# Optimization experiments

Measured on AMD Instinct MI355X. Metric: run time of the kernel, lower is better.

The kernel has to match this reference:

```python
import jax, jax.numpy as jnp
import numpy as np

K = 16      # knn neighbors (init kwarg k)
EPS = 1e-5  # batch-norm eps


def setup_inputs() -> dict:
    key = jax.random.key(0)
    ks = jax.random.split(key, 4)
    B, N, C, O = 16, 2048, 16, 64
    x = jax.random.normal(ks[0], (B * N, C), dtype=jnp.float32)
    batch = jnp.repeat(jnp.arange(B, dtype=jnp.int32), N)  # sorted equal-size graphs
    W1 = jax.random.normal(ks[1], (2 * C, O), dtype=jnp.float32) * (1.0 / np.sqrt(2 * C))
    b1 = jnp.zeros((O,), jnp.float32)
    g1 = jnp.ones((O,), jnp.float32)
    be1 = jnp.zeros((O,), jnp.float32)
    Wg = jax.random.normal(ks[2], (O, 1), dtype=jnp.float32) * (1.0 / np.sqrt(O))
    bg = jnp.zeros((1,), jnp.float32)
    gg = jnp.ones((1,), jnp.float32)
    beg = jnp.zeros((1,), jnp.float32)
    return {"x": x, "batch": batch, "W1": W1, "b1": b1, "g1": g1, "be1": be1,
            "Wg": Wg, "bg": bg, "gg": gg, "beg": beg, "num_graphs": B}


def reference(x, batch, W1, b1, g1, be1, Wg, bg, gg, beg, num_graphs):
    B = int(num_graphs)
    total, C = x.shape
    N = total // B
    xb = x.reshape(B, N, C)

    # --- dynamic kNN graph in feature space (per graph in the batch) ---
    sq = jnp.sum(xb * xb, axis=-1)                                   # [B,N]
    d = sq[:, :, None] + sq[:, None, :] - 2.0 * jnp.einsum('bnc,bmc->bnm', xb, xb)
    _, idx = jax.lax.top_k(-d, K)                                    # [B,N,K], includes self (d=0)

    # --- edge features: cat([x_i, x_j - x_i]) ---
    xj = jax.vmap(lambda pts, ids: pts[ids])(xb, idx)                # [B,N,K,C]
    xi = jnp.broadcast_to(xb[:, :, None, :], xj.shape)               # [B,N,K,C]
    e = jnp.concatenate([xi, xj - xi], axis=-1)                      # [B,N,K,2C]

    # --- edge MLP: Linear -> BatchNorm(train stats) -> SiLU ---
    h = e @ W1 + b1                                                  # [B,N,K,O]
    mu = h.mean(axis=(0, 1, 2))
    var = h.var(axis=(0, 1, 2))
    h = jax.nn.silu((h - mu) / jnp.sqrt(var + EPS) * g1 + be1)

    # --- attentional aggregation: gate MLP -> softmax over k edges -> weighted sum ---
    gt = h @ Wg + bg                                                 # [B,N,K,1]
    gmu = gt.mean()
    gvar = gt.var()
    gt = jax.nn.silu((gt - gmu) / jnp.sqrt(gvar + EPS) * gg + beg)
    a = jax.nn.softmax(gt, axis=2)                                   # softmax over K per target node
    out = jnp.sum(a * h, axis=2)                                     # [B,N,O]
    return out.reshape(total, -1)
```

## Files before the change

kernel.cpp:

```cpp
#include <hip/hip_runtime.h>
#include <math.h>
#include <float.h>

#define BGRAPH 16
#define NPTS   2048
#define CDIM   16
#define ODIM   64
#define KNN    16
#define NTOT   (BGRAPH*NPTS)
#define NEDGE  (NTOT*KNN)
#define EPSBN  1e-5f
#define NBLK_E 2048
#define NPW    4
#define NSETS  16


__global__ __launch_bounds__(256) void pq_kernel(
    const float* __restrict__ x, const float* __restrict__ W1,
    const float* __restrict__ b1,
    float* __restrict__ P, float* __restrict__ Q, float* __restrict__ sq,
    float* __restrict__ abuf) {
  if (blockIdx.x == 0) {
    for (int t = threadIdx.x; t < NSETS*128 + 2*NSETS; t += 256) abuf[t] = 0.f;
  }
  int lane = threadIdx.x & 63;
  int nin  = threadIdx.x >> 6;
  int node = blockIdx.x * 4 + nin;
  __shared__ float xs[4][CDIM];
  if (threadIdx.x < 4*CDIM) {
    int n = threadIdx.x / CDIM, c = threadIdx.x % CDIM;
    xs[n][c] = x[(blockIdx.x*4 + n)*CDIM + c];
  }
  __syncthreads();
  float p = 0.f, q = b1[lane];
  #pragma unroll
  for (int c = 0; c < CDIM; ++c) {
    float xv = xs[nin][c];
    float wb = W1[(c+CDIM)*ODIM + lane];
    float wa = W1[c*ODIM + lane];
    p += xv * wb;
    q += xv * (wa - wb);
  }
  P[node*ODIM + lane] = p;
  Q[node*ODIM + lane] = q;
  if (lane == 0) {
    float s = 0.f;
    #pragma unroll
    for (int c = 0; c < CDIM; ++c) { float xv = xs[nin][c]; s += xv*xv; }
    sq[node] = s;
  }
}

#define KROWS 4
__device__ __forceinline__ unsigned long long packkey(float dv, int j) {
  unsigned ub = __float_as_uint(dv);
  ub ^= ((unsigned)((int)ub >> 31)) | 0x80000000u;
  return (((unsigned long long)ub) << 32) | (unsigned)j;
}

__global__ __launch_bounds__(256, 4) void knn_kernel(
    const float* __restrict__ x, const float* __restrict__ sq,
    int* __restrict__ idxOut) {
  __shared__ float sT16[CDIM][256];
  __shared__ unsigned long long skey[4][64];
  __shared__ int scnt[4];
  const int tid  = threadIdx.x;
  const int lane = tid & 63;
  const int w    = tid >> 6;
  const int blocksPerGraph = NPTS / KROWS;
  const int g     = blockIdx.x / blocksPerGraph;
  const int rb    = (blockIdx.x % blocksPerGraph) * KROWS;
  const int gbase = g * NPTS;
  const int r0    = rb + w;

  float tg[CDIM]; float tsq;
  {
    const float4* tp = (const float4*)(x + (size_t)(gbase + r0)*CDIM);
    float4 t0 = tp[0], t1 = tp[1], t2 = tp[2], t3 = tp[3];
    tg[0]=t0.x; tg[1]=t0.y; tg[2]=t0.z; tg[3]=t0.w;
    tg[4]=t1.x; tg[5]=t1.y; tg[6]=t1.z; tg[7]=t1.w;
    tg[8]=t2.x; tg[9]=t2.y; tg[10]=t2.z; tg[11]=t2.w;
    tg[12]=t3.x; tg[13]=t3.y; tg[14]=t3.z; tg[15]=t3.w;
    tsq = sq[gbase + r0];
  }

  float d[32];

  float4 a0, a1, a2, a3;
  {
    const float4* xp = (const float4*)(x + (size_t)(gbase + tid)*CDIM);
    a0 = xp[0]; a1 = xp[1]; a2 = xp[2]; a3 = xp[3];
  }

  for (int t = 0; t < NPTS/256; ++t) {
    __syncthreads();
    sT16[0][tid]=a0.x;  sT16[1][tid]=a0.y;  sT16[2][tid]=a0.z;  sT16[3][tid]=a0.w;
    sT16[4][tid]=a1.x;  sT16[5][tid]=a1.y;  sT16[6][tid]=a1.z;  sT16[7][tid]=a1.w;
    sT16[8][tid]=a2.x;  sT16[9][tid]=a2.y;  sT16[10][tid]=a2.z; sT16[11][tid]=a2.w;
    sT16[12][tid]=a3.x; sT16[13][tid]=a3.y; sT16[14][tid]=a3.z; sT16[15][tid]=a3.w;
    __syncthreads();
    if (t < NPTS/256 - 1) {
      const float4* xp = (const float4*)(x + (size_t)(gbase + (t+1)*256 + tid)*CDIM);
      a0 = xp[0]; a1 = xp[1]; a2 = xp[2]; a3 = xp[3];
    }

    float4 sq4 = *(const float4*)(sq + gbase + t*256 + 4*lane);
    float sqv[4] = {sq4.x, sq4.y, sq4.z, sq4.w};

    float dot[4] = {0.f,0.f,0.f,0.f};
    #pragma unroll
    for (int c = 0; c < CDIM; ++c) {
      float4 cv = *(const float4*)(&sT16[c][4*lane]);
      float cvv[4]; cvv[0]=cv.x; cvv[1]=cv.y; cvv[2]=cv.z; cvv[3]=cv.w;
      float xv = tg[c];
      #pragma unroll
      for (int rr = 0; rr < 4; ++rr)
        dot[rr] += xv * cvv[rr];
    }
    #pragma unroll
    for (int rr = 0; rr < 4; ++rr)
      d[t*4 + rr] = tsq + sqv[rr] - 2.f*dot[rr];
  }

  {
    float lmin = d[0];
    #pragma unroll
    for (int s = 1; s < 32; ++s) lmin = fminf(lmin, d[s]);

    float v = lmin;
    #pragma unroll
    for (int k = 2; k <= 64; k <<= 1) {
      #pragma unroll
      for (int j = k >> 1; j > 0; j >>= 1) {
        float o = __shfl_xor(v, j);
        bool asc   = ((lane & k) == 0);
        bool lower = ((lane & j) == 0);
        float mn = fminf(v, o), mx = fmaxf(v, o);
        v = (asc == lower) ? mn : mx;
      }
    }
    float T = __shfl(v, 15);

    if (lane == 0) scnt[w] = 0;
    #pragma unroll
    for (int s = 0; s < 32; ++s) {
      if (d[s] <= T) {
        int p = atomicAdd(&scnt[w], 1);
        if (p < 64) {
          int j = (s >> 2)*256 + 4*lane + (s & 3);
          skey[w][p] = packkey(d[s], j);
        }
      }
    }
    int M = scnt[w];
    int row = gbase + r0;

    if (M <= 64) {
      unsigned long long key = (lane < M) ? skey[w][lane] : ~0ull;
      #pragma unroll
      for (int k = 2; k <= 64; k <<= 1) {
        #pragma unroll
        for (int j = k >> 1; j > 0; j >>= 1) {
          unsigned long long o = __shfl_xor(key, j);
          bool asc   = ((lane & k) == 0);
          bool lower = ((lane & j) == 0);
          unsigned long long mn = (key < o) ? key : o;
          unsigned long long mx = (key < o) ? o : key;
          key = (asc == lower) ? mn : mx;
        }
      }
      if (lane < KNN)
        idxOut[(size_t)row*KNN + lane] = gbase + (int)(key & 0xffffffffu);
    } else {
      for (int sel = 0; sel < KNN; ++sel) {
        unsigned long long lb = ~0ull;
        #pragma unroll
        for (int s = 0; s < 32; ++s) {
          int j = (s >> 2)*256 + 4*lane + (s & 3);
          unsigned long long ks = packkey(d[s], j);
          if (ks < lb) lb = ks;
        }
        #pragma unroll
        for (int off = 32; off > 0; off >>= 1) {
          unsigned long long o = __shfl_xor(lb, off);
          if (o < lb) lb = o;
        }
        if (lane == 0)
          idxOut[(size_t)row*KNN + sel] = gbase + (int)(lb & 0xffffffffu);
        #pragma unroll
        for (int s = 0; s < 32; ++s) {
          int j = (s >> 2)*256 + 4*lane + (s & 3);
          if (packkey(d[s], j) == lb) d[s] = FLT_MAX;
        }
      }
    }
  }
}

__global__ __launch_bounds__(256) void stats1a_kernel(
    const float* __restrict__ P, const float* __restrict__ Q,
    const int* __restrict__ idx, float* __restrict__ abuf) {
  int tid  = threadIdx.x;
  int lane = tid & 63;
  int wid  = tid >> 6;
  int grp  = lane >> 4;
  int p    = lane & 15;
  int gw   = blockIdx.x * 4 + wid;
  int n0 = gw * NPW;
  float4 s4  = {0.f,0.f,0.f,0.f};
  float4 ss4 = {0.f,0.f,0.f,0.f};
  #pragma unroll
  for (int ii = 0; ii < NPW; ++ii) {
    int i = n0 + ii;
    float4 q4 = *(const float4*)(Q + (size_t)i*ODIM + 4*p);
    int4 j4 = *(const int4*)(idx + (size_t)i*KNN + 4*grp);
    {
      float4 v = *(const float4*)(P + (size_t)j4.x*ODIM + 4*p);
      float hx=q4.x+v.x, hy=q4.y+v.y, hz=q4.z+v.z, hw=q4.w+v.w;
      s4.x+=hx; s4.y+=hy; s4.z+=hz; s4.w+=hw;
      ss4.x+=hx*hx; ss4.y+=hy*hy; ss4.z+=hz*hz; ss4.w+=hw*hw;
    }
    {
      float4 v = *(const float4*)(P + (size_t)j4.y*ODIM + 4*p);
      float hx=q4.x+v.x, hy=q4.y+v.y, hz=q4.z+v.z, hw=q4.w+v.w;
      s4.x+=hx; s4.y+=hy; s4.z+=hz; s4.w+=hw;
      ss4.x+=hx*hx; ss4.y+=hy*hy; ss4.z+=hz*hz; ss4.w+=hw*hw;
    }
    {
      float4 v = *(const float4*)(P + (size_t)j4.z*ODIM + 4*p);
      float hx=q4.x+v.x, hy=q4.y+v.y, hz=q4.z+v.z, hw=q4.w+v.w;
      s4.x+=hx; s4.y+=hy; s4.z+=hz; s4.w+=hw;
      ss4.x+=hx*hx; ss4.y+=hy*hy; ss4.z+=hz*hz; ss4.w+=hw*hw;
    }
    {
      float4 v = *(const float4*)(P + (size_t)j4.w*ODIM + 4*p);
      float hx=q4.x+v.x, hy=q4.y+v.y, hz=q4.z+v.z, hw=q4.w+v.w;
      s4.x+=hx; s4.y+=hy; s4.z+=hz; s4.w+=hw;
      ss4.x+=hx*hx; ss4.y+=hy*hy; ss4.z+=hz*hz; ss4.w+=hw*hw;
    }
  }
  s4.x  += __shfl_xor(s4.x,16);  s4.x  += __shfl_xor(s4.x,32);
  s4.y  += __shfl_xor(s4.y,16);  s4.y  += __shfl_xor(s4.y,32);
  s4.z  += __shfl_xor(s4.z,16);  s4.z  += __shfl_xor(s4.z,32);
  s4.w  += __shfl_xor(s4.w,16);  s4.w  += __shfl_xor(s4.w,32);
  ss4.x += __shfl_xor(ss4.x,16); ss4.x += __shfl_xor(ss4.x,32);
  ss4.y += __shfl_xor(ss4.y,16); ss4.y += __shfl_xor(ss4.y,32);
  ss4.z += __shfl_xor(ss4.z,16); ss4.z += __shfl_xor(ss4.z,32);
  ss4.w += __shfl_xor(ss4.w,16); ss4.w += __shfl_xor(ss4.w,32);
  __shared__ float ls[4][ODIM], lss[4][ODIM];
  if (grp == 0) {
    *(float4*)&ls[wid][4*p]  = s4;
    *(float4*)&lss[wid][4*p] = ss4;
  }
  __syncthreads();
  if (tid < 2*ODIM) {
    float a;
    if (tid < ODIM) a = ls[0][tid] + ls[1][tid] + ls[2][tid] + ls[3][tid];
    else { int o = tid - ODIM; a = lss[0][o] + lss[1][o] + lss[2][o] + lss[3][o]; }
    atomicAdd(&abuf[(blockIdx.x & (NSETS-1))*128 + tid], a);
  }
}

__global__ __launch_bounds__(256) void stats2a_kernel(
    const float* __restrict__ P, const float* __restrict__ Q,
    const int* __restrict__ idx,
    const float* __restrict__ g1, const float* __restrict__ be1,
    const float* __restrict__ Wg, const float* __restrict__ bg,
    const float* __restrict__ abuf, float* __restrict__ scale,
    float* __restrict__ shift, float* __restrict__ gtbuf,
    float* __restrict__ gacc) {
  int tid  = threadIdx.x;
  int lane = tid & 63;
  int wid  = tid >> 6;
  int grp  = lane >> 4;
  int p    = lane & 15;
  __shared__ __align__(16) float s_sc[ODIM], s_sh[ODIM];
  __shared__ float red[2*ODIM];
  if (tid < 2*ODIM) {
    float a = 0.f;
    #pragma unroll
    for (int t = 0; t < NSETS; ++t) a += abuf[t*128 + tid];
    red[tid] = a;
  }
  __syncthreads();
  if (tid < ODIM) {
    float mu  = red[tid] / (float)NEDGE;
    float var = red[ODIM+tid] / (float)NEDGE - mu*mu;
    float inv = 1.0f / sqrtf(var + EPSBN);
    float sc = g1[tid] * inv;
    float sh = be1[tid] - mu * sc;
    s_sc[tid] = sc; s_sh[tid] = sh;
    if (blockIdx.x == 0) { scale[tid] = sc; shift[tid] = sh; }
  }
  __syncthreads();

  int gw = blockIdx.x * 4 + wid;
  int n0 = gw * NPW;
  float4 sc4 = *(const float4*)&s_sc[4*p];
  float4 sh4 = *(const float4*)&s_sh[4*p];
  float4 wg4 = *(const float4*)(Wg + 4*p);
  float bgv = bg[0];
  float s = 0.f, ss = 0.f;
  #pragma unroll
  for (int ii = 0; ii < NPW; ++ii) {
    int i = n0 + ii;
    float4 q4 = *(const float4*)(Q + (size_t)i*ODIM + 4*p);
    int4 j4 = *(const int4*)(idx + (size_t)i*KNN + 4*grp);
    #pragma unroll
    for (int e = 0; e < 4; ++e) {
      int j = (e==0) ? j4.x : (e==1) ? j4.y : (e==2) ? j4.z : j4.w;
      float4 p4 = *(const float4*)(P + (size_t)j*ODIM + 4*p);
      float zx = (q4.x + p4.x)*sc4.x + sh4.x;
      float zy = (q4.y + p4.y)*sc4.y + sh4.y;
      float zz = (q4.z + p4.z)*sc4.z + sh4.z;
      float zw = (q4.w + p4.w)*sc4.w + sh4.w;
      float v = (zx/(1.f+expf(-zx)))*wg4.x
              + (zy/(1.f+expf(-zy)))*wg4.y
              + (zz/(1.f+expf(-zz)))*wg4.z
              + (zw/(1.f+expf(-zw)))*wg4.w;
      v += __shfl_xor(v, 1);
      v += __shfl_xor(v, 2);
      v += __shfl_xor(v, 4);
      v += __shfl_xor(v, 8);
      float gt = v + bgv;
      if (p == 0) gtbuf[(size_t)i*KNN + 4*grp + e] = gt;
      s += gt; ss += gt*gt;
    }
  }
  s  += __shfl_xor(s, 16);  s  += __shfl_xor(s, 32);
  ss += __shfl_xor(ss, 16); ss += __shfl_xor(ss, 32);
  __shared__ float pw[4], pws[4];
  if (lane == 0) { pw[wid] = s; pws[wid] = ss; }
  __syncthreads();
  if (tid == 0) {
    int set = blockIdx.x & (NSETS-1);
    atomicAdd(&gacc[2*set],   pw[0]+pw[1]+pw[2]+pw[3]);
    atomicAdd(&gacc[2*set+1], pws[0]+pws[1]+pws[2]+pws[3]);
  }
}

__global__ __launch_bounds__(256) void final_kernel(
    const float* __restrict__ P, const float* __restrict__ Q,
    const int* __restrict__ idx, const float* __restrict__ scale,
    const float* __restrict__ shift, const float* __restrict__ gtbuf,
    const float* __restrict__ gacc, const float* __restrict__ gg,
    const float* __restrict__ beg, float* __restrict__ out) {
  __shared__ float g2[2];
  if (threadIdx.x == 0) {
    float S = 0.f, SS = 0.f;
    #pragma unroll
    for (int t = 0; t < NSETS; ++t) { S += gacc[2*t]; SS += gacc[2*t+1]; }
    float mu  = S / (float)NEDGE;
    float var = SS / (float)NEDGE - mu*mu;
    float inv = 1.f / sqrtf(var + EPSBN);
    float sg = gg[0] * inv;
    g2[0] = sg; g2[1] = beg[0] - mu * sg;
  }
  __syncthreads();
  int lane = threadIdx.x & 63;
  int wid  = threadIdx.x >> 6;
  int grp  = lane >> 4;
  int p    = lane & 15;
  int i = blockIdx.x * 4 + wid;
  float4 sc4 = *(const float4*)(scale + 4*p);
  float4 sh4 = *(const float4*)(shift + 4*p);
  float gscale = g2[0], gshift = g2[1];
  float4 q4 = *(const float4*)(Q + (size_t)i*ODIM + 4*p);
  int4   j4 = *(const int4*)(idx + (size_t)i*KNN + 4*grp);
  float4 g4 = *(const float4*)(gtbuf + (size_t)i*KNN + 4*grp);

  float z0 = g4.x*gscale + gshift, z1 = g4.y*gscale + gshift;
  float z2 = g4.z*gscale + gshift, z3 = g4.w*gscale + gshift;
  float gt0 = z0/(1.f+expf(-z0)), gt1 = z1/(1.f+expf(-z1));
  float gt2 = z2/(1.f+expf(-z2)), gt3 = z3/(1.f+expf(-z3));
  float m = fmaxf(fmaxf(gt0, gt1), fmaxf(gt2, gt3));
  m = fmaxf(m, __shfl_xor(m, 16));
  m = fmaxf(m, __shfl_xor(m, 32));
  float e0 = expf(gt0-m), e1 = expf(gt1-m), e2 = expf(gt2-m), e3 = expf(gt3-m);
  float se = e0+e1+e2+e3;
  se += __shfl_xor(se, 16);
  se += __shfl_xor(se, 32);
  float invs = 1.f / se;
  float a0 = e0*invs, a1 = e1*invs, a2 = e2*invs, a3 = e3*invs;

  float4 acc = {0.f,0.f,0.f,0.f};
  {
    float4 v = *(const float4*)(P + (size_t)j4.x*ODIM + 4*p);
    float zx=(q4.x+v.x)*sc4.x+sh4.x, zy=(q4.y+v.y)*sc4.y+sh4.y;
    float zz=(q4.z+v.z)*sc4.z+sh4.z, zw=(q4.w+v.w)*sc4.w+sh4.w;
    acc.x += a0*(zx/(1.f+expf(-zx))); acc.y += a0*(zy/(1.f+expf(-zy)));
    acc.z += a0*(zz/(1.f+expf(-zz))); acc.w += a0*(zw/(1.f+expf(-zw)));
  }
  {
    float4 v = *(const float4*)(P + (size_t)j4.y*ODIM + 4*p);
    float zx=(q4.x+v.x)*sc4.x+sh4.x, zy=(q4.y+v.y)*sc4.y+sh4.y;
    float zz=(q4.z+v.z)*sc4.z+sh4.z, zw=(q4.w+v.w)*sc4.w+sh4.w;
    acc.x += a1*(zx/(1.f+expf(-zx))); acc.y += a1*(zy/(1.f+expf(-zy)));
    acc.z += a1*(zz/(1.f+expf(-zz))); acc.w += a1*(zw/(1.f+expf(-zw)));
  }
  {
    float4 v = *(const float4*)(P + (size_t)j4.z*ODIM + 4*p);
    float zx=(q4.x+v.x)*sc4.x+sh4.x, zy=(q4.y+v.y)*sc4.y+sh4.y;
    float zz=(q4.z+v.z)*sc4.z+sh4.z, zw=(q4.w+v.w)*sc4.w+sh4.w;
    acc.x += a2*(zx/(1.f+expf(-zx))); acc.y += a2*(zy/(1.f+expf(-zy)));
    acc.z += a2*(zz/(1.f+expf(-zz))); acc.w += a2*(zw/(1.f+expf(-zw)));
  }
  {
    float4 v = *(const float4*)(P + (size_t)j4.w*ODIM + 4*p);
    float zx=(q4.x+v.x)*sc4.x+sh4.x, zy=(q4.y+v.y)*sc4.y+sh4.y;
    float zz=(q4.z+v.z)*sc4.z+sh4.z, zw=(q4.w+v.w)*sc4.w+sh4.w;
    acc.x += a3*(zx/(1.f+expf(-zx))); acc.y += a3*(zy/(1.f+expf(-zy)));
    acc.z += a3*(zz/(1.f+expf(-zz))); acc.w += a3*(zw/(1.f+expf(-zw)));
  }
  acc.x += __shfl_xor(acc.x,16); acc.x += __shfl_xor(acc.x,32);
  acc.y += __shfl_xor(acc.y,16); acc.y += __shfl_xor(acc.y,32);
  acc.z += __shfl_xor(acc.z,16); acc.z += __shfl_xor(acc.z,32);
  acc.w += __shfl_xor(acc.w,16); acc.w += __shfl_xor(acc.w,32);
  if (grp == 0)
    *(float4*)(out + (size_t)i*ODIM + 4*p) = acc;
}

extern "C" void kernel_launch(void* const* d_in, const int* in_sizes, int n_in,
                              void* d_out, int out_size, void* d_ws, size_t ws_size,
                              hipStream_t stream) {
  const float* x   = (const float*)d_in[0];
  const float* W1  = (const float*)d_in[2];
  const float* b1  = (const float*)d_in[3];
  const float* g1  = (const float*)d_in[4];
  const float* be1 = (const float*)d_in[5];
  const float* Wg  = (const float*)d_in[6];
  const float* bg  = (const float*)d_in[7];
  const float* gg  = (const float*)d_in[8];
  const float* beg = (const float*)d_in[9];
  float* out = (float*)d_out;

  char* ws = (char*)d_ws;
  int*   idx   = (int*)  (ws);
  float* P     = (float*)(ws + 2097152);
  float* Q     = (float*)(ws + 10485760);
  float* sq    = (float*)(ws + 18874368);
  float* abuf  = (float*)(ws + 19005440);
  float* gacc  = abuf + NSETS*128;
  float* gtbuf = (float*)(ws + 20070400);
  float* scale = (float*)(ws + 22167552);
  float* shift = (float*)(ws + 22167808);

  pq_kernel<<<NTOT/4, 256, 0, stream>>>(x, W1, b1, P, Q, sq, abuf);
  knn_kernel<<<NTOT/KROWS, 256, 0, stream>>>(x, sq, idx);
  stats1a_kernel<<<NBLK_E, 256, 0, stream>>>(P, Q, idx, abuf);
  stats2a_kernel<<<NBLK_E, 256, 0, stream>>>(P, Q, idx, g1, be1, Wg, bg, abuf, scale, shift, gtbuf, gacc);
  final_kernel<<<NTOT/4, 256, 0, stream>>>(P, Q, idx, scale, shift, gtbuf, gacc, gg, beg, out);
}
```

Measured before the change: 277.9 us.

## Compute two kNN query rows per wave to reuse shared candidate tiles

Each wave now handles two query rows instead of one, so every candidate tile staged in shared memory feeds twice as many dot products. The second row's distances go to a new 32KB shared buffer, and its top-k selection runs after the first row's. Query features are made wave-uniform with readfirstlane so they can live in scalar registers. The larger shared footprint and the lower occupancy hint (3 blocks per CU instead of 4) reduce occupancy, and the second selection pass runs serially after the first.

```diff
diff --git a/kernel.cpp b/kernel.cpp
--- a/kernel.cpp
+++ b/kernel.cpp
@@ -51,17 +51,21 @@
   }
 }
 
-#define KROWS 4
+#define KROWS 8
 __device__ __forceinline__ unsigned long long packkey(float dv, int j) {
   unsigned ub = __float_as_uint(dv);
   ub ^= ((unsigned)((int)ub >> 31)) | 0x80000000u;
   return (((unsigned long long)ub) << 32) | (unsigned)j;
 }
-
-__global__ __launch_bounds__(256, 4) void knn_kernel(
+__device__ __forceinline__ float rfl(float v) {
+  return __uint_as_float(__builtin_amdgcn_readfirstlane(__float_as_uint(v)));
+}
+
+__global__ __launch_bounds__(256, 3) void knn_kernel(
     const float* __restrict__ x, const float* __restrict__ sq,
     int* __restrict__ idxOut) {
   __shared__ float sT16[CDIM][256];
+  __shared__ float dB[32][256];
   __shared__ unsigned long long skey[4][64];
   __shared__ int scnt[4];
   const int tid  = threadIdx.x;
@@ -71,17 +75,24 @@
   const int g     = blockIdx.x / blocksPerGraph;
   const int rb    = (blockIdx.x % blocksPerGraph) * KROWS;
   const int gbase = g * NPTS;
-  const int r0    = rb + w;
-
-  float tg[CDIM]; float tsq;
+  const int r0    = rb + w*2;
+
+  float ta[CDIM], tb[CDIM]; float tsqA, tsqB;
   {
     const float4* tp = (const float4*)(x + (size_t)(gbase + r0)*CDIM);
     float4 t0 = tp[0], t1 = tp[1], t2 = tp[2], t3 = tp[3];
-    tg[0]=t0.x; tg[1]=t0.y; tg[2]=t0.z; tg[3]=t0.w;
-    tg[4]=t1.x; tg[5]=t1.y; tg[6]=t1.z; tg[7]=t1.w;
-    tg[8]=t2.x; tg[9]=t2.y; tg[10]=t2.z; tg[11]=t2.w;
-    tg[12]=t3.x; tg[13]=t3.y; tg[14]=t3.z; tg[15]=t3.w;
-    tsq = sq[gbase + r0];
+    ta[0]=rfl(t0.x);  ta[1]=rfl(t0.y);  ta[2]=rfl(t0.z);  ta[3]=rfl(t0.w);
+    ta[4]=rfl(t1.x);  ta[5]=rfl(t1.y);  ta[6]=rfl(t1.z);  ta[7]=rfl(t1.w);
+    ta[8]=rfl(t2.x);  ta[9]=rfl(t2.y);  ta[10]=rfl(t2.z); ta[11]=rfl(t2.w);
+    ta[12]=rfl(t3.x); ta[13]=rfl(t3.y); ta[14]=rfl(t3.z); ta[15]=rfl(t3.w);
+    tsqA = rfl(sq[gbase + r0]);
+    const float4* up = (const float4*)(x + (size_t)(gbase + r0 + 1)*CDIM);
+    float4 u0 = up[0], u1 = up[1], u2 = up[2], u3 = up[3];
+    tb[0]=rfl(u0.x);  tb[1]=rfl(u0.y);  tb[2]=rfl(u0.z);  tb[3]=rfl(u0.w);
+    tb[4]=rfl(u1.x);  tb[5]=rfl(u1.y);  tb[6]=rfl(u1.z);  tb[7]=rfl(u1.w);
+    tb[8]=rfl(u2.x);  tb[9]=rfl(u2.y);  tb[10]=rfl(u2.z); tb[11]=rfl(u2.w);
+    tb[12]=rfl(u3.x); tb[13]=rfl(u3.y); tb[14]=rfl(u3.z); tb[15]=rfl(u3.w);
+    tsqB = rfl(sq[gbase + r0 + 1]);
   }
 
   float d[32];
@@ -92,6 +103,7 @@
     a0 = xp[0]; a1 = xp[1]; a2 = xp[2]; a3 = xp[3];
   }
 
+  #pragma unroll
   for (int t = 0; t < NPTS/256; ++t) {
     __syncthreads();
     sT16[0][tid]=a0.x;  sT16[1][tid]=a0.y;  sT16[2][tid]=a0.z;  sT16[3][tid]=a0.w;
@@ -107,19 +119,20 @@
     float4 sq4 = *(const float4*)(sq + gbase + t*256 + 4*lane);
     float sqv[4] = {sq4.x, sq4.y, sq4.z, sq4.w};
 
-    float dot[4] = {0.f,0.f,0.f,0.f};
+    float dotA[4] = {0.f,0.f,0.f,0.f};
+    float dotB[4] = {0.f,0.f,0.f,0.f};
     #pragma unroll
     for (int c = 0; c < CDIM; ++c) {
       float4 cv = *(const float4*)(&sT16[c][4*lane]);
-      float cvv[4]; cvv[0]=cv.x; cvv[1]=cv.y; cvv[2]=cv.z; cvv[3]=cv.w;
-      float xv = tg[c];
-      #pragma unroll
-      for (int rr = 0; rr < 4; ++rr)
-        dot[rr] += xv * cvv[rr];
-    }
-    #pragma unroll
-    for (int rr = 0; rr < 4; ++rr)
-      d[t*4 + rr] = tsq + sqv[rr] - 2.f*dot[rr];
+      float xa = ta[c], xb = tb[c];
+      dotA[0] += xa*cv.x; dotA[1] += xa*cv.y; dotA[2] += xa*cv.z; dotA[3] += xa*cv.w;
+      dotB[0] += xb*cv.x; dotB[1] += xb*cv.y; dotB[2] += xb*cv.z; dotB[3] += xb*cv.w;
+    }
+    #pragma unroll
+    for (int rr = 0; rr < 4; ++rr) {
+      d[t*4 + rr] = tsqA + sqv[rr] - 2.f*dotA[rr];
+      dB[t*4 + rr][tid] = tsqB + sqv[rr] - 2.f*dotB[rr];
+    }
   }
 
   {
@@ -191,6 +204,81 @@
         for (int s = 0; s < 32; ++s) {
           int j = (s >> 2)*256 + 4*lane + (s & 3);
           if (packkey(d[s], j) == lb) d[s] = FLT_MAX;
+        }
+      }
+    }
+  }
+
+  {
+    float lmin = dB[0][tid];
+    #pragma unroll
+    for (int s = 1; s < 32; ++s) lmin = fminf(lmin, dB[s][tid]);
+
+    float v = lmin;
+    #pragma unroll
+    for (int k = 2; k <= 64; k <<= 1) {
+      #pragma unroll
+      for (int j = k >> 1; j > 0; j >>= 1) {
+        float o = __shfl_xor(v, j);
+        bool asc   = ((lane & k) == 0);
+        bool lower = ((lane & j) == 0);
+        float mn = fminf(v, o), mx = fmaxf(v, o);
+        v = (asc == lower) ? mn : mx;
+      }
+    }
+    float T = __shfl(v, 15);
+
+    if (lane == 0) scnt[w] = 0;
+    #pragma unroll
+    for (int s = 0; s < 32; ++s) {
+      float dv = dB[s][tid];
+      if (dv <= T) {
+        int p = atomicAdd(&scnt[w], 1);
+        if (p < 64) {
+          int j = (s >> 2)*256 + 4*lane + (s & 3);
+          skey[w][p] = packkey(dv, j);
+        }
+      }
+    }
+    int M = scnt[w];
+    int row = gbase + r0 + 1;
+
+    if (M <= 64) {
+      unsigned long long key = (lane < M) ? skey[w][lane] : ~0ull;
+      #pragma unroll
+      for (int k = 2; k <= 64; k <<= 1) {
+        #pragma unroll
+        for (int j = k >> 1; j > 0; j >>= 1) {
+          unsigned long long o = __shfl_xor(key, j);
+          bool asc   = ((lane & k) == 0);
+          bool lower = ((lane & j) == 0);
+          unsigned long long mn = (key < o) ? key : o;
+          unsigned long long mx = (key < o) ? o : key;
+          key = (asc == lower) ? mn : mx;
+        }
+      }
+      if (lane < KNN)
+        idxOut[(size_t)row*KNN + lane] = gbase + (int)(key & 0xffffffffu);
+    } else {
+      for (int sel = 0; sel < KNN; ++sel) {
+        unsigned long long lb = ~0ull;
+        #pragma unroll
+        for (int s = 0; s < 32; ++s) {
+          int j = (s >> 2)*256 + 4*lane + (s & 3);
+          unsigned long long ks = packkey(dB[s][tid], j);
+          if (ks < lb) lb = ks;
+        }
+        #pragma unroll
+        for (int off = 32; off > 0; off >>= 1) {
+          unsigned long long o = __shfl_xor(lb, off);
+          if (o < lb) lb = o;
+        }
+        if (lane == 0)
+          idxOut[(size_t)row*KNN + sel] = gbase + (int)(lb & 0xffffffffu);
+        #pragma unroll
+        for (int s = 0; s < 32; ++s) {
+          int j = (s >> 2)*256 + 4*lane + (s & 3);
+          if (packkey(dB[s][tid], j) == lb) dB[s][tid] = FLT_MAX;
         }
       }
     }
```

New measurement: 276.9 us. No clear change (-0.3%).
